# Kernel optimization log

Hardware: AMD Instinct MI355X
Metric: run time of the kernel (lower is better)

Reference implementation:

```python
import jax, jax.numpy as jnp
import numpy as np

N_NODES = 100000
N_EDGES = 3200000
D_IN = 256
H1 = 16
H2 = 32


def _xavier(key, shape):
    fan_in, fan_out = shape
    a = jnp.sqrt(6.0 / (fan_in + fan_out))
    return jax.random.uniform(key, shape, jnp.float32, -a, a)


def setup_inputs() -> dict:
    key = jax.random.key(0)
    ks = jax.random.split(key, 8)
    x = jax.random.normal(ks[0], (N_NODES, D_IN), jnp.float32)
    edge_rows = jax.random.randint(ks[1], (N_EDGES,), 0, N_NODES, jnp.int32)
    edge_cols = jax.random.randint(ks[2], (N_EDGES,), 0, N_NODES, jnp.int32)
    edge_vals = jax.random.uniform(ks[3], (N_EDGES,), jnp.float32)
    W1 = _xavier(ks[4], (D_IN, H1))
    W2 = _xavier(ks[5], (H1, H2))
    w_out = _xavier(ks[6], (H2, 1))
    b_out = jnp.zeros((1,), jnp.float32)
    return {"x": x, "edge_vals": edge_vals, "W1": W1, "W2": W2,
            "w_out": w_out, "b_out": b_out,
            "edge_rows": edge_rows, "edge_cols": edge_cols}


def _spmm(edge_rows, edge_cols, edge_vals, dense):
    # out[i] = sum_{e: row[e]==i} val[e] * dense[col[e]]  == torch.spmm(adj, dense)
    gathered = dense[edge_cols] * edge_vals[:, None]  # [E, F]
    return jax.ops.segment_sum(gathered, edge_rows, num_segments=N_NODES)


def reference(x, edge_vals, W1, W2, w_out, b_out, edge_rows, edge_cols):
    # gc1: mm -> spmm -> relu (dropout=0)
    h = jax.nn.relu(_spmm(edge_rows, edge_cols, edge_vals, x @ W1))  # [N, H1]
    # gc2: mm -> spmm -> identity
    z = _spmm(edge_rows, edge_cols, edge_vals, h @ W2)  # [N, H2]
    z_pooled = jnp.sum(z, axis=0)  # [H2]
    out = jax.nn.sigmoid(z_pooled @ w_out + b_out)  # [1]
    return out
```

## Files before the change

### kernel.cpp

```cpp
#include <hip/hip_runtime.h>
#include <math.h>

#define N_NODES 100000
#define D_IN 256
#define H1 16
#define H2 32
#define NT1 1563

static __device__ __forceinline__ float bf_lo(unsigned int u) {
    return __uint_as_float(u << 16);
}
static __device__ __forceinline__ float bf_hi(unsigned int u) {
    return __uint_as_float(u & 0xffff0000u);
}
static __device__ __forceinline__ unsigned int f2bf_rne(float f) {
    unsigned int u = __float_as_uint(f);
    return (u + 0x7fffu + ((u >> 16) & 1u)) >> 16;
}
static __device__ __forceinline__ unsigned int pack_bf16(float lo, float hi) {
    return f2bf_rne(lo) | (f2bf_rne(hi) << 16);
}
static __device__ __forceinline__ unsigned int cvt_pk_bf16(float lo, float hi) {
    unsigned int r;
    asm("v_cvt_pk_bf16_f32 %0, %1, %2" : "=v"(r) : "v"(lo), "v"(hi));
    return r;
}

typedef __attribute__((ext_vector_type(8))) short bf16x8;
typedef __attribute__((ext_vector_type(4))) float f32x4;
union ABFrag { unsigned int u[4]; bf16x8 v; };

__global__ __launch_bounds__(256) void k_xw1z(const float* __restrict__ x,
                                              const float* __restrict__ W1,
                                              unsigned short* __restrict__ t,
                                              float4* __restrict__ g2z,
                                              float* __restrict__ s,
                                              unsigned int* __restrict__ flag) {
    const int tid = threadIdx.x;
    const int bid = blockIdx.x;

    int zi = bid * 256 + tid;
    if (zi < 200000) g2z[zi] = make_float4(0.f, 0.f, 0.f, 0.f);
    if (bid == 0) {
        if (tid < 16) s[tid] = 0.f;
        if (tid == 16) *flag = 0u;
    }

    const int lane = tid & 63;
    const int wid  = tid >> 6;
    const int fcol = lane & 15;
    const int kgrp = lane >> 4;

    ABFrag bfrag[8];
#pragma unroll
    for (int g = 0; g < 8; g++) {
        const float* wp = W1 + (g * 32 + kgrp * 8) * H1 + fcol;
#pragma unroll
        for (int p = 0; p < 4; p++)
            bfrag[g].u[p] = cvt_pk_bf16(wp[(2 * p) * H1], wp[(2 * p + 1) * H1]);
    }

    const int row0 = bid * 64 + wid * 16;
    int arow = row0 + fcol;
    if (arow >= N_NODES) arow = N_NODES - 1;
    const float* xr = x + (size_t)arow * D_IN;
    f32x4 acc = {0.f, 0.f, 0.f, 0.f};
#pragma unroll
    for (int g = 0; g < 8; g++) {
        const float4 a0 = *(const float4*)(xr + g * 32 + kgrp * 8);
        const float4 a1 = *(const float4*)(xr + g * 32 + kgrp * 8 + 4);
        ABFrag af;
        af.u[0] = cvt_pk_bf16(a0.x, a0.y);
        af.u[1] = cvt_pk_bf16(a0.z, a0.w);
        af.u[2] = cvt_pk_bf16(a1.x, a1.y);
        af.u[3] = cvt_pk_bf16(a1.z, a1.w);
        acc = __builtin_amdgcn_mfma_f32_16x16x32_bf16(af.v, bfrag[g].v, acc, 0, 0, 0);
    }
#pragma unroll
    for (int r = 0; r < 4; r++) {
        int orow = row0 + kgrp * 4 + r;
        if (orow < N_NODES)
            t[(size_t)orow * H1 + fcol] = (unsigned short)f2bf_rne(acc[r]);
    }
}

__global__ __launch_bounds__(256) void k_edge(const int* __restrict__ rows,
                                              const int* __restrict__ cols,
                                              const float* __restrict__ vals,
                                              const unsigned int* __restrict__ tb,
                                              unsigned int* __restrict__ g2, int E) {
    int tid = blockIdx.x * 256 + threadIdx.x;
    int e = tid >> 3;
    int f2 = tid & 7;
    if (e >= E) return;
    int r = rows[e];
    int c = cols[e];
    float v = vals[e];
    unsigned int tv = tb[c * 8 + f2];
    unsigned int pk = pack_bf16(v * bf_lo(tv), v * bf_hi(tv));
    unsigned int* addr = g2 + (r * 8 + f2);
    asm volatile("global_atomic_pk_add_bf16 %0, %1, off"
                 :: "v"(addr), "v"(pk) : "memory");
}

__global__ __launch_bounds__(256) void k_s2out(const int* __restrict__ cols,
                                               const float* __restrict__ vals,
                                               const unsigned int* __restrict__ g2,
                                               float* __restrict__ s,
                                               unsigned int* __restrict__ flag,
                                               const float* __restrict__ W2,
                                               const float* __restrict__ w_out,
                                               const float* __restrict__ b_out,
                                               float* __restrict__ out, int E) {
    const int tid = threadIdx.x;
    const int f2 = tid & 7;
    int idx    = (blockIdx.x * 256 + tid) >> 3;
    int stride = (gridDim.x * 256) >> 3;
    float accl = 0.f, acch = 0.f;
    for (int e = idx; e < E; e += stride) {
        int c = cols[e];
        float v = vals[e];
        unsigned int gv = g2[c * 8 + f2];
        accl = fmaf(v, fmaxf(bf_lo(gv), 0.f), accl);
        acch = fmaf(v, fmaxf(bf_hi(gv), 0.f), acch);
    }
    accl += __shfl_xor(accl, 8, 64);
    accl += __shfl_xor(accl, 16, 64);
    accl += __shfl_xor(accl, 32, 64);
    acch += __shfl_xor(acch, 8, 64);
    acch += __shfl_xor(acch, 16, 64);
    acch += __shfl_xor(acch, 32, 64);
    __shared__ float red[4][16];
    __shared__ int slast;
    int lane = tid & 63, wid = tid >> 6;
    if (lane < 8) { red[wid][2 * lane] = accl; red[wid][2 * lane + 1] = acch; }
    __syncthreads();
    if (tid < 16) {
        float v = red[0][tid] + red[1][tid] + red[2][tid] + red[3][tid];
        atomicAdd(&s[tid], v);
    }
    if (tid == 0) {
        __threadfence();
        unsigned int old = atomicAdd(flag, 1u);
        slast = (old == gridDim.x - 1) ? 1 : 0;
    }
    __syncthreads();
    if (slast && tid < 64) {
        float sv = (tid < H1) ? atomicAdd(&s[tid], 0.f) : 0.f;
        float m = 0.f;
        if (tid < H2) {
            float v = 0.f;
#pragma unroll
            for (int f1 = 0; f1 < H1; f1++)
                v = fmaf(__shfl(sv, f1, 64), W2[f1 * H2 + tid], v);
            m = v * w_out[tid];
        }
        for (int off = 32; off; off >>= 1) m += __shfl_down(m, off, 64);
        if (tid == 0) out[0] = 1.f / (1.f + expf(-(m + b_out[0])));
    }
}

extern "C" void kernel_launch(void* const* d_in, const int* in_sizes, int n_in,
                              void* d_out, int out_size, void* d_ws, size_t ws_size,
                              hipStream_t stream) {
    const float* x         = (const float*)d_in[0];
    const float* edge_vals = (const float*)d_in[1];
    const float* W1        = (const float*)d_in[2];
    const float* W2        = (const float*)d_in[3];
    const float* w_out     = (const float*)d_in[4];
    const float* b_out     = (const float*)d_in[5];
    const int*   edge_rows = (const int*)d_in[6];
    const int*   edge_cols = (const int*)d_in[7];
    float* out = (float*)d_out;

    const int E = in_sizes[1];

    char* ws = (char*)d_ws;
    unsigned short* t    = (unsigned short*)(ws);
    unsigned int*   g2   = (unsigned int*)(ws + 3200000);
    float*          s    = (float*)(ws + 6400000);
    unsigned int*   flag = (unsigned int*)(ws + 6400128);

    k_xw1z<<<NT1, 256, 0, stream>>>(x, W1, t, (float4*)g2, s, flag);

    long long edge_threads = (long long)E * 8;
    k_edge<<<(int)((edge_threads + 255) / 256), 256, 0, stream>>>(
        edge_rows, edge_cols, edge_vals, (const unsigned int*)t, g2, E);

    k_s2out<<<1024, 256, 0, stream>>>(edge_cols, edge_vals, g2, s, flag,
                                      W2, w_out, b_out, out, E);
}
```

Measured before the change: 412.9 us.

## Bin edges by destination row block and accumulate in LDS

Replaces the per-edge global bf16 atomic scatter with a counting-sort pipeline on every call. A histogram kernel, a scan and a scatter kernel group edges into 64-row buckets as packed (col, row-offset, value) records. A new kernel then accumulates each bucket into shared memory with fp32 atomics and issues one packed bf16 global atomic per row and feature pair. The aim is to cut random global atomic traffic and contention, at the cost of extra passes over the edge arrays and about 25 MB of workspace writes. The old per-edge kernel stays as a fallback when the workspace is too small.

```diff
diff --git a/kernel.cpp b/kernel.cpp
--- a/kernel.cpp
+++ b/kernel.cpp
@@ -6,6 +6,11 @@
 #define H1 16
 #define H2 32
 #define NT1 1563
+#define BSHIFT 6
+#define BROWS 64
+#define NB 1563
+#define CH 8192
+#define GSPLIT 4
 
 static __device__ __forceinline__ float bf_lo(unsigned int u) {
     return __uint_as_float(u << 16);
@@ -33,18 +38,12 @@
 __global__ __launch_bounds__(256) void k_xw1z(const float* __restrict__ x,
                                               const float* __restrict__ W1,
                                               unsigned short* __restrict__ t,
-                                              float4* __restrict__ g2z,
-                                              float* __restrict__ s,
-                                              unsigned int* __restrict__ flag) {
+                                              float4* __restrict__ zero4) {
     const int tid = threadIdx.x;
     const int bid = blockIdx.x;
 
     int zi = bid * 256 + tid;
-    if (zi < 200000) g2z[zi] = make_float4(0.f, 0.f, 0.f, 0.f);
-    if (bid == 0) {
-        if (tid < 16) s[tid] = 0.f;
-        if (tid == 16) *flag = 0u;
-    }
+    if (zi < 200464) zero4[zi] = make_float4(0.f, 0.f, 0.f, 0.f);
 
     const int lane = tid & 63;
     const int wid  = tid >> 6;
@@ -84,23 +83,122 @@
     }
 }
 
-__global__ __launch_bounds__(256) void k_edge(const int* __restrict__ rows,
-                                              const int* __restrict__ cols,
-                                              const float* __restrict__ vals,
+__global__ __launch_bounds__(256) void k_hist(const int* __restrict__ rows,
+                                              int* __restrict__ hist, int E) {
+    __shared__ int lh[NB];
+    int tid = threadIdx.x;
+    for (int b = tid; b < NB; b += 256) lh[b] = 0;
+    __syncthreads();
+    int stride = gridDim.x * 256;
+    for (int i = blockIdx.x * 256 + tid; i < E; i += stride)
+        atomicAdd(&lh[rows[i] >> BSHIFT], 1);
+    __syncthreads();
+    for (int b = tid; b < NB; b += 256) {
+        int c = lh[b];
+        if (c) atomicAdd(&hist[b], c);
+    }
+}
+
+__global__ __launch_bounds__(256) void k_scan(const int* __restrict__ hist,
+                                              int* __restrict__ base,
+                                              unsigned int* __restrict__ cursor) {
+    __shared__ int scan[256];
+    int tid = threadIdx.x;
+    int loc[7]; int mysum = 0;
+#pragma unroll
+    for (int j = 0; j < 7; j++) {
+        int b = tid * 7 + j;
+        int h = (b < NB) ? hist[b] : 0;
+        loc[j] = mysum; mysum += h;
+    }
+    scan[tid] = mysum;
+    __syncthreads();
+    int incl = mysum;
+    for (int off = 1; off < 256; off <<= 1) {
+        int add = (tid >= off) ? scan[tid - off] : 0;
+        __syncthreads();
+        incl += add; scan[tid] = incl;
+        __syncthreads();
+    }
+    int excl = incl - mysum;
+#pragma unroll
+    for (int j = 0; j < 7; j++) {
+        int b = tid * 7 + j;
+        if (b < NB) {
+            int v = excl + loc[j];
+            base[b] = v;
+            cursor[b * 8] = (unsigned int)v;
+        }
+    }
+    if (tid == 255) base[NB] = incl;
+}
+
+__global__ __launch_bounds__(256) void k_scatter(const int* __restrict__ rows,
+                                                 const int* __restrict__ cols,
+                                                 const float* __restrict__ vals,
+                                                 unsigned int* __restrict__ cursor,
+                                                 uint2* __restrict__ ed, int E) {
+    __shared__ int lcount[NB];
+    __shared__ int lbase[NB];
+    int tid = threadIdx.x;
+    int c0 = blockIdx.x * CH;
+    int cend = min(c0 + CH, E);
+    for (int b = tid; b < NB; b += 256) lcount[b] = 0;
+    __syncthreads();
+    for (int i = c0 + tid; i < cend; i += 256)
+        atomicAdd(&lcount[rows[i] >> BSHIFT], 1);
+    __syncthreads();
+    for (int b = tid; b < NB; b += 256) {
+        int c = lcount[b];
+        lbase[b] = c ? (int)atomicAdd(&cursor[b * 8], (unsigned int)c) : 0;
+        lcount[b] = 0;
+    }
+    __syncthreads();
+    for (int i = c0 + tid; i < cend; i += 256) {
+        int r = rows[i];
+        int b = r >> BSHIFT;
+        int rank = atomicAdd(&lcount[b], 1);
+        int pos = lbase[b] + rank;
+        ed[pos] = make_uint2(((unsigned int)cols[i] << BSHIFT) |
+                                 (unsigned int)(r & (BROWS - 1)),
+                             __float_as_uint(vals[i]));
+    }
+}
+
+__global__ __launch_bounds__(256) void k_gacc(const uint2* __restrict__ ed,
+                                              const int* __restrict__ base,
                                               const unsigned int* __restrict__ tb,
-                                              unsigned int* __restrict__ g2, int E) {
-    int tid = blockIdx.x * 256 + threadIdx.x;
-    int e = tid >> 3;
-    int f2 = tid & 7;
-    if (e >= E) return;
-    int r = rows[e];
-    int c = cols[e];
-    float v = vals[e];
-    unsigned int tv = tb[c * 8 + f2];
-    unsigned int pk = pack_bf16(v * bf_lo(tv), v * bf_hi(tv));
-    unsigned int* addr = g2 + (r * 8 + f2);
-    asm volatile("global_atomic_pk_add_bf16 %0, %1, off"
-                 :: "v"(addr), "v"(pk) : "memory");
+                                              unsigned int* __restrict__ g2) {
+    __shared__ float gs[BROWS * H1];
+    const int tid = threadIdx.x;
+    const int bb = blockIdx.x >> 2;
+    const int j  = blockIdx.x & (GSPLIT - 1);
+    for (int i = tid; i < BROWS * H1; i += 256) gs[i] = 0.f;
+    __syncthreads();
+    const int e0 = base[bb], e1 = base[bb + 1];
+    const int len = e1 - e0;
+    const int es = e0 + ((len * j) >> 2);
+    const int ee = e0 + ((len * (j + 1)) >> 2);
+    const int f2 = tid & 7, grp = tid >> 3;
+    for (int i = es + grp; i < ee; i += 32) {
+        uint2 e = ed[i];
+        int c  = (int)(e.x >> BSHIFT);
+        int r6 = (int)(e.x & (BROWS - 1));
+        float v = __uint_as_float(e.y);
+        unsigned int tv = tb[c * 8 + f2];
+        atomicAdd(&gs[r6 * H1 + 2 * f2],     v * bf_lo(tv));
+        atomicAdd(&gs[r6 * H1 + 2 * f2 + 1], v * bf_hi(tv));
+    }
+    __syncthreads();
+    const int row0 = bb << BSHIFT;
+    for (int idx = tid; idx < BROWS * 8; idx += 256) {
+        int row = idx >> 3, fp = idx & 7;
+        unsigned int pk = pack_bf16(gs[row * H1 + 2 * fp],
+                                    gs[row * H1 + 2 * fp + 1]);
+        unsigned int* addr = g2 + (size_t)(row0 + row) * 8 + fp;
+        asm volatile("global_atomic_pk_add_bf16 %0, %1, off"
+                     :: "v"(addr), "v"(pk) : "memory");
+    }
 }
 
 __global__ __launch_bounds__(256) void k_s2out(const int* __restrict__ cols,
@@ -160,6 +258,25 @@
     }
 }
 
+__global__ __launch_bounds__(256) void k_edge(const int* __restrict__ rows,
+                                              const int* __restrict__ cols,
+                                              const float* __restrict__ vals,
+                                              const unsigned int* __restrict__ tb,
+                                              unsigned int* __restrict__ g2, int E) {
+    int tid = blockIdx.x * 256 + threadIdx.x;
+    int e = tid >> 3;
+    int f2 = tid & 7;
+    if (e >= E) return;
+    int r = rows[e];
+    int c = cols[e];
+    float v = vals[e];
+    unsigned int tv = tb[c * 8 + f2];
+    unsigned int pk = pack_bf16(v * bf_lo(tv), v * bf_hi(tv));
+    unsigned int* addr = g2 + (r * 8 + f2);
+    asm volatile("global_atomic_pk_add_bf16 %0, %1, off"
+                 :: "v"(addr), "v"(pk) : "memory");
+}
+
 extern "C" void kernel_launch(void* const* d_in, const int* in_sizes, int n_in,
                               void* d_out, int out_size, void* d_ws, size_t ws_size,
                               hipStream_t stream) {
@@ -178,14 +295,28 @@
     char* ws = (char*)d_ws;
     unsigned short* t    = (unsigned short*)(ws);
     unsigned int*   g2   = (unsigned int*)(ws + 3200000);
-    float*          s    = (float*)(ws + 6400000);
-    unsigned int*   flag = (unsigned int*)(ws + 6400128);
-
-    k_xw1z<<<NT1, 256, 0, stream>>>(x, W1, t, (float4*)g2, s, flag);
-
-    long long edge_threads = (long long)E * 8;
-    k_edge<<<(int)((edge_threads + 255) / 256), 256, 0, stream>>>(
-        edge_rows, edge_cols, edge_vals, (const unsigned int*)t, g2, E);
+    float*          s    = (float*)(ws + 6401024);
+    unsigned int*   flag = (unsigned int*)(ws + 6401088);
+    int*            hist = (int*)(ws + 6401152);
+    int*            base = (int*)(ws + 6407424);
+    unsigned int*   cur  = (unsigned int*)(ws + 6413696);
+    uint2*          ed   = (uint2*)(ws + 6463744);
+
+    k_xw1z<<<NT1, 256, 0, stream>>>(x, W1, t, (float4*)(ws + 3200000));
+
+    bool binned = (ws_size >= 32063744) && (E <= 3200000);
+    if (binned) {
+        k_hist<<<256, 256, 0, stream>>>(edge_rows, hist, E);
+        k_scan<<<1, 256, 0, stream>>>(hist, base, cur);
+        k_scatter<<<(E + CH - 1) / CH, 256, 0, stream>>>(
+            edge_rows, edge_cols, edge_vals, cur, ed, E);
+        k_gacc<<<NB * GSPLIT, 256, 0, stream>>>(ed, base,
+                                                (const unsigned int*)t, g2);
+    } else {
+        long long edge_threads = (long long)E * 8;
+        k_edge<<<(int)((edge_threads + 255) / 256), 256, 0, stream>>>(
+            edge_rows, edge_cols, edge_vals, (const unsigned int*)t, g2, E);
+    }
 
     k_s2out<<<1024, 256, 0, stream>>>(edge_cols, edge_vals, g2, s, flag,
                                       W2, w_out, b_out, out, E);
```

Measured after the change: 650.6 us. 57.6% more time.
